# Optimization experiments

Measured on AMD Instinct MI355X. Metric: run time of the kernel, lower is better.

The kernel has to match this reference:

```python
import jax, jax.numpy as jnp
import numpy as np

D = 1024
E = 8
K = 2
NUM_ITER = 2
DT = 0.1
H = 64           # controller_hidden
CTX = 2 * D


def _gelu(t):
    return jax.nn.gelu(t, approximate=False)


def _inl(ctrl, x, v, mu):
    # ctrl: [T, 3D] -> alpha, beta, gate chunks of size D
    alpha_raw, beta_raw, gate_raw = jnp.split(ctrl, 3, axis=-1)
    alpha = jax.nn.sigmoid(alpha_raw)
    beta = jax.nn.softplus(beta_raw)
    gate = jax.nn.sigmoid(gate_raw)
    error = x - mu
    v_next = alpha * v - beta * error
    x_next = x + DT * gate * v_next
    return x_next, v_next


def setup_inputs() -> dict:
    key = jax.random.key(0)
    ks = jax.random.split(key, 20)
    s = 0.02
    inp = {
        'x': jax.random.normal(ks[0], (4, 4096, D), jnp.float32),
        # router MLP
        'w_r1': jax.random.normal(ks[1], (D, D // 4), jnp.float32) * s,
        'b_r1': jnp.zeros((D // 4,), jnp.float32),
        'w_r2': jax.random.normal(ks[2], (D // 4, E), jnp.float32) * s,
        'b_r2': jnp.zeros((E,), jnp.float32),
        # halt gate MLP
        'w_h1': jax.random.normal(ks[3], (D, D // 4), jnp.float32) * s,
        'b_h1': jnp.zeros((D // 4,), jnp.float32),
        'w_h2': jax.random.normal(ks[4], (D // 4, 1), jnp.float32) * s,
        'b_h2': jnp.zeros((1,), jnp.float32),
        # expert tables
        'expert_w1': jax.random.normal(ks[5], (E, CTX, H), jnp.float32) * s,
        'expert_b1': jnp.zeros((E, H), jnp.float32),
        'expert_w2': jax.random.normal(ks[6], (E, H, 3 * D), jnp.float32) * s,
        'expert_b2': jnp.zeros((E, 3 * D), jnp.float32),
        # shared expert
        'w_s1': jax.random.normal(ks[7], (CTX, H), jnp.float32) * s,
        'b_s1': jnp.zeros((H,), jnp.float32),
        'w_s2': jax.random.normal(ks[8], (H, 3 * D), jnp.float32) * s,
        'b_s2': jnp.zeros((3 * D,), jnp.float32),
        'shared_weight': jnp.asarray(0.5, jnp.float32),
        # refine MLP
        'w_f1': jax.random.normal(ks[9], (D, 2 * D), jnp.float32) * s,
        'b_f1': jnp.zeros((2 * D,), jnp.float32),
        'w_f2': jax.random.normal(ks[10], (2 * D, D), jnp.float32) * s,
        'b_f2': jnp.zeros((D,), jnp.float32),
        'integration_weight': jnp.full((D,), 0.5, jnp.float32),
        'mu': jnp.zeros((D,), jnp.float32),
    }
    return inp


def reference(x, w_r1, b_r1, w_r2, b_r2, w_h1, b_h1, w_h2, b_h2,
              expert_w1, expert_b1, expert_w2, expert_b2,
              w_s1, b_s1, w_s2, b_s2, shared_weight,
              w_f1, b_f1, w_f2, b_f2, integration_weight, mu):
    B, N, Dm = x.shape
    xf = x.reshape(B * N, Dm)                       # [T, D]

    # router: top-k over softmax probs, renormalized
    logits = _gelu(xf @ w_r1 + b_r1) @ w_r2 + b_r2  # [T, E]
    probs = jax.nn.softmax(logits, axis=-1)
    top_p, top_i = jax.lax.top_k(probs, K)          # [T, K]
    top_p = top_p / jnp.sum(top_p, axis=-1, keepdims=True)

    flat_idx = top_i.reshape(-1)                    # [T*K]
    flat_w = top_p.reshape(-1, 1)                   # [T*K, 1]

    v = jnp.zeros_like(xf)
    integrated = xf
    for _ in range(NUM_ITER):
        ctx = jnp.concatenate([integrated, v], axis=-1)     # [T, 2D]

        # shared expert path
        shared_ctrl = _gelu(ctx @ w_s1 + b_s1) @ w_s2 + b_s2
        x_shared, v_shared = _inl(shared_ctrl, integrated, v, mu)
        sw = jax.nn.sigmoid(shared_weight)

        # routed experts: gather per-token weights, per-token matvec
        ctx_e = jnp.repeat(ctx, K, axis=0)                  # [T*K, 2D]
        x_e = jnp.repeat(integrated, K, axis=0)
        v_e = jnp.repeat(v, K, axis=0)
        w1 = expert_w1[flat_idx]                            # [T*K, 2D, H]
        b1 = expert_b1[flat_idx]
        w2 = expert_w2[flat_idx]                            # [T*K, H, 3D]
        b2 = expert_b2[flat_idx]
        hidden = _gelu(jnp.einsum('tc,tch->th', ctx_e, w1) + b1)
        ctrl = jnp.einsum('th,tho->to', hidden, w2) + b2    # [T*K, 3D]
        x_r, v_r = _inl(ctrl, x_e, v_e, mu)
        x_r = (x_r * flat_w).reshape(B * N, K, Dm).sum(axis=1)
        v_r = (v_r * flat_w).reshape(B * N, K, Dm).sum(axis=1)

        x_next = sw * x_shared + (1.0 - sw) * x_r
        v_next = sw * v_shared + (1.0 - sw) * v_r

        halt = jax.nn.sigmoid(_gelu(x_next @ w_h1 + b_h1) @ w_h2 + b_h2)  # [T,1]
        refined = _gelu(x_next @ w_f1 + b_f1) @ w_f2 + b_f2               # [T,D]
        integrated = integrated + halt * refined * integration_weight
        v = v_next

    return integrated.reshape(B, N, Dm)
```

## Files before the change

kernel.cpp:

```cpp
#include <hip/hip_runtime.h>


#define TOK   16384
#define DDIM  1024
#define NEXP  8
#define DTC   0.1f
#define MAXDESC 512
#define NDBLK 392

using f32x4 = __attribute__((ext_vector_type(4))) float;
using bfv8  = __attribute__((ext_vector_type(8))) short;

__device__ __forceinline__ unsigned short f2bf(float x){
  unsigned u = __builtin_bit_cast(unsigned, x);
  u += 0x7fffu + ((u >> 16) & 1u);
  return (unsigned short)(u >> 16);
}
__device__ __forceinline__ float bf2f(unsigned short h){
  return __builtin_bit_cast(float, ((unsigned)h) << 16);
}
__device__ __forceinline__ float geluf(float x){
  return 0.5f * x * (1.0f + erff(x * 0.7071067811865476f));
}
__device__ __forceinline__ float sigmf(float x){ return 1.0f/(1.0f+__expf(-x)); }
__device__ __forceinline__ float softpf(float x){
  return fmaxf(x, 0.0f) + __logf(1.0f + __expf(-fabsf(x)));
}
__device__ __forceinline__ f32x4 mfma16(bfv8 a, bfv8 b, f32x4 c){
  return __builtin_amdgcn_mfma_f32_16x16x32_bf16(a, b, c, 0, 0, 0);
}
typedef __attribute__((address_space(1))) const void gvoid_t;
typedef __attribute__((address_space(3))) void svoid_t;
__device__ __forceinline__ void gload16(const void* g, void* l){
  __builtin_amdgcn_global_load_lds((gvoid_t*)g, (svoid_t*)l, 16, 0, 0);
}

__global__ __launch_bounds__(256) void transpose_cast(
    const float* __restrict__ src, unsigned short* __restrict__ dst, int R, int C)
{
  __shared__ float tile[32][33];
  size_t bo = (size_t)blockIdx.z * R * C;
  const float* s = src + bo;
  unsigned short* d = dst + bo;
  int c0 = blockIdx.x * 32, r0 = blockIdx.y * 32;
  int tx = threadIdx.x, ty = threadIdx.y;
  #pragma unroll
  for (int j = 0; j < 4; j++)
    tile[ty + 8*j][tx] = s[(size_t)(r0 + ty + 8*j) * C + c0 + tx];
  __syncthreads();
  #pragma unroll
  for (int j = 0; j < 4; j++)
    d[(size_t)(c0 + ty + 8*j) * R + r0 + tx] = f2bf(tile[tx][ty + 8*j]);
}

template<bool INIT>
__global__ __launch_bounds__(256) void ctx_k(
    const float* __restrict__ outf, unsigned short* __restrict__ ctx)
{
  const int n = TOK * 256;
  for (int i = blockIdx.x * 256 + threadIdx.x; i < n; i += gridDim.x * 256) {
    int t = i >> 8, c4 = (i & 255) * 4;
    float4 xi = ((const float4*)outf)[i];
    ushort4 xb = {f2bf(xi.x), f2bf(xi.y), f2bf(xi.z), f2bf(xi.w)};
    *(ushort4*)&ctx[(size_t)t*2048 + c4] = xb;
    if (INIT)
      *(ushort4*)&ctx[(size_t)t*2048 + 1024 + c4] = ushort4{0,0,0,0};
  }
}

template<int EPI>
__global__ __launch_bounds__(256) void gemm_k(
    const unsigned short* __restrict__ A, int lda,
    const unsigned short* __restrict__ BT,
    const float* __restrict__ bias, int Kd, int N,
    unsigned short* __restrict__ obf,
    const float* __restrict__ halt, const float* __restrict__ iw,
    float* __restrict__ integ)
{
  __shared__ unsigned short As[128][64];
  __shared__ unsigned short Bs[128][64];
  const int tid  = threadIdx.x, lane = tid & 63, w = tid >> 6;
  const int wm   = w >> 1, wn = w & 1;
  const int gm0  = blockIdx.y * 128, gn0 = blockIdx.x * 128;
  const int r8   = lane >> 3;
  const int sseg = (lane & 7) ^ r8;

  const unsigned short* aga[4];
  const unsigned short* bga[4];
  #pragma unroll
  for (int c = 0; c < 4; c++) {
    aga[c] = A  + (size_t)(gm0 + w*32 + c*8 + r8) * lda + sseg*8;
    bga[c] = BT + (size_t)(gn0 + w*32 + c*8 + r8) * Kd  + sseg*8;
  }

  f32x4 acc[4][4];
  #pragma unroll
  for (int i = 0; i < 4; i++)
    #pragma unroll
    for (int j = 0; j < 4; j++)
      acc[i][j] = f32x4{0.f,0.f,0.f,0.f};

  const int xr = (lane & 7) << 3;
  for (int k0 = 0; k0 < Kd; k0 += 64) {
    #pragma unroll
    for (int c = 0; c < 4; c++) gload16(aga[c] + k0, &As[w*32 + c*8][0]);
    #pragma unroll
    for (int c = 0; c < 4; c++) gload16(bga[c] + k0, &Bs[w*32 + c*8][0]);
    __syncthreads();
    #pragma unroll
    for (int kk = 0; kk < 64; kk += 32) {
      const int kof = kk + ((lane >> 4) << 3);
      bfv8 a[4], b[4];
      #pragma unroll
      for (int mf = 0; mf < 4; mf++)
        a[mf] = *(const bfv8*)&As[wm*64 + mf*16 + (lane & 15)][kof ^ xr];
      #pragma unroll
      for (int nf = 0; nf < 4; nf++)
        b[nf] = *(const bfv8*)&Bs[wn*64 + nf*16 + (lane & 15)][kof ^ xr];
      #pragma unroll
      for (int mf = 0; mf < 4; mf++)
        #pragma unroll
        for (int nf = 0; nf < 4; nf++)
          acc[mf][nf] = mfma16(a[mf], b[nf], acc[mf][nf]);
    }
    __syncthreads();
  }

  #pragma unroll
  for (int mf = 0; mf < 4; mf++) {
    #pragma unroll
    for (int nf = 0; nf < 4; nf++) {
      int col = gn0 + wn*64 + nf*16 + (lane & 15);
      float bc = bias[col];
      #pragma unroll
      for (int r = 0; r < 4; r++) {
        int row = gm0 + wm*64 + mf*16 + ((lane >> 4) << 2) + r;
        float v = acc[mf][nf][r] + bc;
        if (EPI == 0) {
          obf[(size_t)row * N + col] = f2bf(geluf(v));
        } else {
          integ[(size_t)row * DDIM + col] += halt[row] * v * iw[col];
        }
      }
    }
  }
}

__global__ __launch_bounds__(256) void router_k(
    const unsigned short* __restrict__ h1, const float* __restrict__ w_r2,
    const float* __restrict__ b_r2, int* __restrict__ topi, float* __restrict__ topw)
{
  int t = blockIdx.x * 4 + (threadIdx.x >> 6);
  int lane = threadIdx.x & 63;
  const unsigned short* hp = h1 + (size_t)t * 256 + lane * 4;
  float hv[4];
  #pragma unroll
  for (int j = 0; j < 4; j++) hv[j] = bf2f(hp[j]);
  float acc[8];
  #pragma unroll
  for (int e = 0; e < 8; e++) acc[e] = 0.f;
  #pragma unroll
  for (int j = 0; j < 4; j++) {
    const float* wr = w_r2 + (size_t)(lane*4 + j) * 8;
    #pragma unroll
    for (int e = 0; e < 8; e++) acc[e] += hv[j] * wr[e];
  }
  #pragma unroll
  for (int off = 32; off > 0; off >>= 1)
    #pragma unroll
    for (int e = 0; e < 8; e++) acc[e] += __shfl_xor(acc[e], off);
  if (lane == 0) {
    float lg[8];
    #pragma unroll
    for (int e = 0; e < 8; e++) lg[e] = acc[e] + b_r2[e];
    int i0 = 0; float m0 = lg[0];
    #pragma unroll
    for (int e = 1; e < 8; e++) if (lg[e] > m0) { m0 = lg[e]; i0 = e; }
    int i1 = -1; float m1 = -3.4e38f;
    #pragma unroll
    for (int e = 0; e < 8; e++) if (e != i0 && lg[e] > m1) { m1 = lg[e]; i1 = e; }
    float w0 = 1.0f / (1.0f + expf(m1 - m0));
    topi[t*2] = i0; topi[t*2+1] = i1;
    topw[t*2] = w0; topw[t*2+1] = 1.0f - w0;
  }
}

__global__ __launch_bounds__(256) void haltgate_k(
    const unsigned short* __restrict__ h1, const float* __restrict__ w_h2,
    const float* __restrict__ b_h2, float* __restrict__ halt)
{
  int t = blockIdx.x * 4 + (threadIdx.x >> 6);
  int lane = threadIdx.x & 63;
  const unsigned short* hp = h1 + (size_t)t * 256 + lane * 4;
  float s = 0.f;
  #pragma unroll
  for (int j = 0; j < 4; j++) s += bf2f(hp[j]) * w_h2[lane*4 + j];
  #pragma unroll
  for (int off = 32; off > 0; off >>= 1) s += __shfl_xor(s, off);
  if (lane == 0) halt[t] = sigmf(s + b_h2[0]);
}

__global__ __launch_bounds__(256) void bucket_k(
    const int* __restrict__ topi, int* __restrict__ cnt, int* __restrict__ slots)
{
  int g = blockIdx.x * 256 + threadIdx.x;
  int e = topi[g];
  int p = atomicAdd(&cnt[e], 1);
  slots[e * 32768 + p] = g;
}

__global__ void desc_k(const int* __restrict__ cnt, int4* __restrict__ desc,
                       int* __restrict__ ndesc)
{
  if (threadIdx.x == 0 && blockIdx.x == 0) {
    int nt = 0, hb = 0;
    for (int e = 0; e <= 8; e++) {
      int c = (e < 8) ? cnt[e] : TOK;
      for (int o = 0; o < c; o += 128) {
        int rem = c - o; if (rem > 128) rem = 128;
        desc[nt] = make_int4(e, o, rem, hb);
        nt++; hb += 128;
      }
    }
    ndesc[0] = nt;
  }
}

__global__ __launch_bounds__(256) void exp1_k(
    const unsigned short* __restrict__ ctx,
    const int4* __restrict__ desc, const int* __restrict__ ndesc,
    const int* __restrict__ slots,
    const unsigned short* __restrict__ ew1T, const float* __restrict__ eb1,
    const unsigned short* __restrict__ ws1T, const float* __restrict__ bs1,
    unsigned short* __restrict__ hiddenG)
{
  __shared__ unsigned short As[128][64];
  __shared__ unsigned short Bs[64][64];
  __shared__ int s_tok[128];
  if (blockIdx.x >= ndesc[0]) return;
  int4 dd = desc[blockIdx.x];
  const int e = dd.x, goff = dd.y, cnt = dd.z, hbase = dd.w;
  const unsigned short* w1 = (e < 8) ? ew1T + (size_t)e * 64 * 2048 : ws1T;
  const float* b1 = (e < 8) ? eb1 + e * 64 : bs1;
  const int tid = threadIdx.x, lane = tid & 63, w = tid >> 6;

  if (tid < 128) {
    int tok;
    if (e < 8) tok = (tid < cnt) ? (slots[e * 32768 + goff + tid] >> 1) : 0;
    else       tok = goff + tid;
    s_tok[tid] = tok;
  }
  __syncthreads();

  const int arow = w*8 + (lane >> 3);
  const int sseg = (lane & 7) ^ (lane >> 3);
  const unsigned short* asrc[4];
  #pragma unroll
  for (int q = 0; q < 4; q++)
    asrc[q] = ctx + (size_t)s_tok[q*32 + arow] * 2048 + sseg * 8;
  const unsigned short* bsrc[2];
  #pragma unroll
  for (int q = 0; q < 2; q++)
    bsrc[q] = w1 + (size_t)(q*32 + arow) * 2048 + sseg * 8;

  f32x4 acc[2][4];
  #pragma unroll
  for (int i = 0; i < 2; i++)
    #pragma unroll
    for (int j = 0; j < 4; j++)
      acc[i][j] = f32x4{0.f,0.f,0.f,0.f};

  const int xr = (lane & 7) << 3;
  for (int k0 = 0; k0 < 2048; k0 += 64) {
    #pragma unroll
    for (int q = 0; q < 4; q++) gload16(asrc[q] + k0, &As[q*32 + w*8][0]);
    #pragma unroll
    for (int q = 0; q < 2; q++) gload16(bsrc[q] + k0, &Bs[q*32 + w*8][0]);
    __syncthreads();
    #pragma unroll
    for (int kk = 0; kk < 64; kk += 32) {
      const int kof = kk + ((lane >> 4) << 3);
      bfv8 a[2], b[4];
      #pragma unroll
      for (int mf = 0; mf < 2; mf++)
        a[mf] = *(const bfv8*)&As[w*32 + mf*16 + (lane & 15)][kof ^ xr];
      #pragma unroll
      for (int nf = 0; nf < 4; nf++)
        b[nf] = *(const bfv8*)&Bs[nf*16 + (lane & 15)][kof ^ xr];
      #pragma unroll
      for (int mf = 0; mf < 2; mf++)
        #pragma unroll
        for (int nf = 0; nf < 4; nf++)
          acc[mf][nf] = mfma16(a[mf], b[nf], acc[mf][nf]);
    }
    __syncthreads();
  }

  #pragma unroll
  for (int mf = 0; mf < 2; mf++) {
    #pragma unroll
    for (int nf = 0; nf < 4; nf++) {
      int col = nf*16 + (lane & 15);
      float bb = b1[col];
      #pragma unroll
      for (int r = 0; r < 4; r++) {
        int row = w*32 + mf*16 + ((lane >> 4) << 2) + r;
        hiddenG[(size_t)(hbase + row) * 64 + col] = f2bf(geluf(acc[mf][nf][r] + bb));
      }
    }
  }
}

__global__ __launch_bounds__(256) void exp2_k(
    const unsigned short* __restrict__ hiddenG,
    const int4* __restrict__ desc, const int* __restrict__ ndesc,
    const int* __restrict__ slots, const float* __restrict__ topw,
    const unsigned short* __restrict__ ew2T, const float* __restrict__ eb2,
    const unsigned short* __restrict__ ws2T, const float* __restrict__ bs2,
    const float* __restrict__ swp, const float* __restrict__ mu,
    const unsigned short* __restrict__ ctx,
    unsigned* __restrict__ padPK, int dhalf)
{
  __shared__ unsigned short Hs[128][64];
  __shared__ unsigned short W2s[192][64];
  __shared__ int   s_tok[128];
  __shared__ int   s_sid[128];
  __shared__ float s_cw[128];
  if (blockIdx.x >= ndesc[0]) return;
  int4 dd = desc[blockIdx.x];
  const int e = dd.x, goff = dd.y, cnt = dd.z, hbase = dd.w;
  const unsigned short* w2 = (e < 8) ? ew2T + (size_t)e * 3072 * 64 : ws2T;
  const float* b2 = (e < 8) ? eb2 + e * 3072 : bs2;
  const int tid = threadIdx.x, lane = tid & 63, w = tid >> 6;
  const float sw = sigmf(swp[0]);

  if (tid < 128) {
    int tok = 0, sid = -1; float cw = 0.f;
    if (e < 8) {
      if (tid < cnt) { int s = slots[e*32768 + goff + tid]; tok = s >> 1; sid = s; cw = (1.f - sw) * topw[s]; }
    } else { tok = goff + tid; sid = 32768 + tok; cw = sw; }
    s_tok[tid] = tok; s_sid[tid] = sid; s_cw[tid] = cw;
  }
  const int arow = w*8 + (lane >> 3);
  const int sseg = (lane & 7) ^ (lane >> 3);
  #pragma unroll
  for (int q = 0; q < 4; q++)
    gload16(hiddenG + (size_t)(hbase + q*32 + arow) * 64 + sseg*8, &Hs[q*32 + w*8][0]);
  __syncthreads();

  const int xr = (lane & 7) << 3;
  bfv8 afr[2][2];
  #pragma unroll
  for (int mf = 0; mf < 2; mf++)
    #pragma unroll
    for (int kk = 0; kk < 2; kk++) {
      int r = w*32 + mf*16 + (lane & 15);
      int kof = kk*32 + ((lane >> 4) << 3);
      afr[mf][kk] = *(const bfv8*)&Hs[r][kof ^ xr];
    }

  for (int dc = 0; dc < 8; dc++) {
    const int d00 = dhalf * 512 + dc * 64;
    #pragma unroll
    for (int q = 0; q < 6; q++) {
      int row  = q*32 + arow;
      int grow = (row >> 6) * 1024 + d00 + (row & 63);
      gload16(w2 + (size_t)grow * 64 + sseg*8, &W2s[q*32 + w*8][0]);
    }
    __syncthreads();

    f32x4 acc[2][12];
    #pragma unroll
    for (int i = 0; i < 2; i++)
      #pragma unroll
      for (int j = 0; j < 12; j++)
        acc[i][j] = f32x4{0.f,0.f,0.f,0.f};
    #pragma unroll
    for (int kk = 0; kk < 2; kk++) {
      const int kof = kk*32 + ((lane >> 4) << 3);
      #pragma unroll
      for (int nf = 0; nf < 12; nf++) {
        bfv8 b = *(const bfv8*)&W2s[nf*16 + (lane & 15)][kof ^ xr];
        acc[0][nf] = mfma16(afr[0][kk], b, acc[0][nf]);
        acc[1][nf] = mfma16(afr[1][kk], b, acc[1][nf]);
      }
    }

    #pragma unroll
    for (int mf = 0; mf < 2; mf++) {
      #pragma unroll
      for (int cf = 0; cf < 4; cf++) {
        int d = d00 + cf*16 + (lane & 15);
        float ba = b2[d], bb = b2[1024 + d], bg = b2[2048 + d];
        float muv = mu[d];
        #pragma unroll
        for (int r = 0; r < 4; r++) {
          int row = w*32 + mf*16 + ((lane >> 4) << 2) + r;
          if (row >= cnt) continue;
          float cw = s_cw[row]; int tok = s_tok[row];
          float al = sigmf(acc[mf][cf][r] + ba);
          float be = softpf(acc[mf][4 + cf][r] + bb);
          float ga = sigmf(acc[mf][8 + cf][r] + bg);
          float xx = bf2f(ctx[(size_t)tok*2048 + d]);
          float vv = bf2f(ctx[(size_t)tok*2048 + 1024 + d]);
          float vn = al * vv - be * (xx - muv);
          unsigned pk = (unsigned)f2bf(cw * vn) | ((unsigned)f2bf(cw * ga * vn) << 16);
          padPK[(size_t)s_sid[row] * 512 + (d - dhalf*512)] = pk;
        }
      }
    }
    __syncthreads();
  }
}

__global__ __launch_bounds__(256) void combine_k(
    const unsigned* __restrict__ padPK, unsigned short* __restrict__ ctx,
    unsigned short* __restrict__ xaccB, int dhalf)
{
  const int n = TOK * 128;
  const uint4* p4 = (const uint4*)padPK;
  for (int i = blockIdx.x * 256 + threadIdx.x; i < n; i += gridDim.x * 256) {
    int t = i >> 7, j = i & 127;
    int gd = dhalf*512 + j*4;
    uint4 p0 = p4[(size_t)(2*t)       * 128 + j];
    uint4 p1 = p4[(size_t)(2*t + 1)   * 128 + j];
    uint4 ps = p4[(size_t)(32768 + t) * 128 + j];
    ushort4 xs = *(const ushort4*)&ctx[(size_t)t*2048 + gd];
    unsigned pc[4][3] = {{p0.x,p1.x,ps.x},{p0.y,p1.y,ps.y},{p0.z,p1.z,ps.z},{p0.w,p1.w,ps.w}};
    unsigned short xi[4] = {xs.x, xs.y, xs.z, xs.w};
    ushort4 xo, vo;
    unsigned short* xop = (unsigned short*)&xo;
    unsigned short* vop = (unsigned short*)&vo;
    #pragma unroll
    for (int k = 0; k < 4; k++) {
      float v  = bf2f((unsigned short)(pc[k][0] & 0xffff))
               + bf2f((unsigned short)(pc[k][1] & 0xffff))
               + bf2f((unsigned short)(pc[k][2] & 0xffff));
      float gv = bf2f((unsigned short)(pc[k][0] >> 16))
               + bf2f((unsigned short)(pc[k][1] >> 16))
               + bf2f((unsigned short)(pc[k][2] >> 16));
      float x = bf2f(xi[k]);
      xop[k] = f2bf(x + DTC * gv);
      vop[k] = f2bf(v);
    }
    *(ushort4*)&xaccB[(size_t)t*1024 + gd]      = xo;
    *(ushort4*)&ctx[(size_t)t*2048 + 1024 + gd] = vo;
  }
}

extern "C" void kernel_launch(void* const* d_in, const int* in_sizes, int n_in,
                              void* d_out, int out_size, void* d_ws, size_t ws_size,
                              hipStream_t stream)
{
  const float* x    = (const float*)d_in[0];
  const float* w_r1 = (const float*)d_in[1];
  const float* b_r1 = (const float*)d_in[2];
  const float* w_r2 = (const float*)d_in[3];
  const float* b_r2 = (const float*)d_in[4];
  const float* w_h1 = (const float*)d_in[5];
  const float* b_h1 = (const float*)d_in[6];
  const float* w_h2 = (const float*)d_in[7];
  const float* b_h2 = (const float*)d_in[8];
  const float* ew1  = (const float*)d_in[9];
  const float* eb1  = (const float*)d_in[10];
  const float* ew2  = (const float*)d_in[11];
  const float* eb2  = (const float*)d_in[12];
  const float* w_s1 = (const float*)d_in[13];
  const float* b_s1 = (const float*)d_in[14];
  const float* w_s2 = (const float*)d_in[15];
  const float* b_s2 = (const float*)d_in[16];
  const float* swt  = (const float*)d_in[17];
  const float* w_f1 = (const float*)d_in[18];
  const float* b_f1 = (const float*)d_in[19];
  const float* w_f2 = (const float*)d_in[20];
  const float* b_f2 = (const float*)d_in[21];
  const float* iw   = (const float*)d_in[22];
  const float* mu   = (const float*)d_in[23];
  float* out = (float*)d_out;

  char* ws = (char*)d_ws;
  size_t off = 0;
  auto take = [&](size_t bytes) -> char* {
    char* p = ws + off;
    off = (off + bytes + 255) & ~(size_t)255;
    return p;
  };
  const size_t TD4 = (size_t)TOK * DDIM * 4;
  unsigned short* xaccB = (unsigned short*)take((size_t)TOK * 1024 * 2);
  unsigned short* ctx   = (unsigned short*)take((size_t)TOK * 2048 * 2);
  unsigned* padPK = (unsigned*)take((size_t)49152 * 512 * 4);
  unsigned short* rh = (unsigned short*)padPK;
  unsigned short* hiddenG = (unsigned short*)take((size_t)NDBLK * 128 * 64 * 2);
  unsigned short* h1 = (unsigned short*)take((size_t)TOK * 256 * 2);
  float* halt = (float*)take((size_t)TOK * 4);
  int*   topi = (int*)take((size_t)TOK * 2 * 4);
  float* topw = (float*)take((size_t)TOK * 2 * 4);
  int*   cnt  = (int*)take(64);
  int*   ndsc = (int*)take(64);
  int4*  desc = (int4*)take((size_t)MAXDESC * 16);
  int*   slots= (int*)take((size_t)NEXP * 32768 * 4);
  unsigned short* w_r1T = (unsigned short*)take((size_t)256 * 1024 * 2);
  unsigned short* w_h1T = (unsigned short*)take((size_t)256 * 1024 * 2);
  unsigned short* w_f1T = (unsigned short*)take((size_t)2048 * 1024 * 2);
  unsigned short* w_f2T = (unsigned short*)take((size_t)1024 * 2048 * 2);
  unsigned short* w_s1T = (unsigned short*)take((size_t)64 * 2048 * 2);
  unsigned short* w_s2T = (unsigned short*)take((size_t)3072 * 64 * 2);
  unsigned short* ew1T  = (unsigned short*)take((size_t)NEXP * 64 * 2048 * 2);
  unsigned short* ew2T  = (unsigned short*)take((size_t)NEXP * 3072 * 64 * 2);
  if (off > ws_size) return;

  hipMemcpyAsync(out, x, TD4, hipMemcpyDeviceToDevice, stream);
  hipMemsetAsync(cnt, 0, 64, stream);

  dim3 tb(32, 8);
  transpose_cast<<<dim3(  8, 32, 1), tb, 0, stream>>>(w_r1, w_r1T, 1024,  256);
  transpose_cast<<<dim3(  8, 32, 1), tb, 0, stream>>>(w_h1, w_h1T, 1024,  256);
  transpose_cast<<<dim3( 64, 32, 1), tb, 0, stream>>>(w_f1, w_f1T, 1024, 2048);
  transpose_cast<<<dim3( 32, 64, 1), tb, 0, stream>>>(w_f2, w_f2T, 2048, 1024);
  transpose_cast<<<dim3(  2, 64, 1), tb, 0, stream>>>(w_s1, w_s1T, 2048,   64);
  transpose_cast<<<dim3( 96,  2, 1), tb, 0, stream>>>(w_s2, w_s2T,   64, 3072);
  transpose_cast<<<dim3(  2, 64, 8), tb, 0, stream>>>(ew1,  ew1T,  2048,   64);
  transpose_cast<<<dim3( 96,  2, 8), tb, 0, stream>>>(ew2,  ew2T,    64, 3072);

  ctx_k<true><<<2048, 256, 0, stream>>>(out, ctx);
  gemm_k<0><<<dim3(2, 128), 256, 0, stream>>>(
      ctx, 2048, w_r1T, b_r1, 1024, 256, h1, nullptr, nullptr, nullptr);
  router_k<<<TOK / 4, 256, 0, stream>>>(h1, w_r2, b_r2, topi, topw);
  bucket_k<<<TOK * 2 / 256, 256, 0, stream>>>(topi, cnt, slots);
  desc_k<<<1, 64, 0, stream>>>(cnt, desc, ndsc);

  for (int it = 0; it < 2; it++) {
    if (it > 0)
      ctx_k<false><<<2048, 256, 0, stream>>>(out, ctx);
    exp1_k<<<NDBLK, 256, 0, stream>>>(ctx, desc, ndsc, slots,
                                      ew1T, eb1, w_s1T, b_s1, hiddenG);
    for (int h = 0; h < 2; h++) {
      exp2_k<<<NDBLK, 256, 0, stream>>>(hiddenG, desc, ndsc, slots, topw,
                                        ew2T, eb2, w_s2T, b_s2, swt, mu,
                                        ctx, padPK, h);
      combine_k<<<2048, 256, 0, stream>>>(padPK, ctx, xaccB, h);
    }
    gemm_k<0><<<dim3(2, 128), 256, 0, stream>>>(
        xaccB, 1024, w_h1T, b_h1, 1024, 256, h1, nullptr, nullptr, nullptr);
    haltgate_k<<<TOK / 4, 256, 0, stream>>>(h1, w_h2, b_h2, halt);
    gemm_k<0><<<dim3(16, 128), 256, 0, stream>>>(
        xaccB, 1024, w_f1T, b_f1, 1024, 2048, rh, nullptr, nullptr, nullptr);
    gemm_k<1><<<dim3(8, 128), 256, 0, stream>>>(
        rh, 2048, w_f2T, b_f2, 2048, 1024, nullptr, halt, iw, out);
  }
}
```

Measured before the change: 1.389 ms.

## Fuse shared expert with combine, merge halt/refine GEMMs, emit ctx from epilogue

The shared-expert second layer moves into its own kernel that also does the combine step: it reads the routed padPK partials and writes xaccB and v directly, so the separate combine pass and the shared-expert padPK rows are dropped. The halt and refine first-layer weights are concatenated so one GEMM (EPI 2) writes both outputs. The refine-output GEMM epilogue now writes the bf16 copy of the updated state into ctx, which removes the per-iteration ctx_k pass. A block-index swizzle is also added to gemm_k to improve L2 locality. The cost is more scattered epilogue loads in the fused shared kernel.

After: 1.557 ms. +12.1%, slower.

```diff
diff --git a/kernel.cpp b/kernel.cpp
--- a/kernel.cpp
+++ b/kernel.cpp
@@ -7,6 +7,7 @@
 #define DTC   0.1f
 #define MAXDESC 512
 #define NDBLK 392
+#define SHBASE 33664
 
 using f32x4 = __attribute__((ext_vector_type(4))) float;
 using bfv8  = __attribute__((ext_vector_type(8))) short;
@@ -53,7 +54,6 @@
     d[(size_t)(c0 + ty + 8*j) * R + r0 + tx] = f2bf(tile[tx][ty + 8*j]);
 }
 
-template<bool INIT>
 __global__ __launch_bounds__(256) void ctx_k(
     const float* __restrict__ outf, unsigned short* __restrict__ ctx)
 {
@@ -63,8 +63,7 @@
     float4 xi = ((const float4*)outf)[i];
     ushort4 xb = {f2bf(xi.x), f2bf(xi.y), f2bf(xi.z), f2bf(xi.w)};
     *(ushort4*)&ctx[(size_t)t*2048 + c4] = xb;
-    if (INIT)
-      *(ushort4*)&ctx[(size_t)t*2048 + 1024 + c4] = ushort4{0,0,0,0};
+    *(ushort4*)&ctx[(size_t)t*2048 + 1024 + c4] = ushort4{0,0,0,0};
   }
 }
 
@@ -72,16 +71,22 @@
 __global__ __launch_bounds__(256) void gemm_k(
     const unsigned short* __restrict__ A, int lda,
     const unsigned short* __restrict__ BT,
-    const float* __restrict__ bias, int Kd, int N,
-    unsigned short* __restrict__ obf,
+    const float* __restrict__ bias, const float* __restrict__ bias2,
+    int Kd, int N,
+    unsigned short* __restrict__ obf, unsigned short* __restrict__ obf2,
     const float* __restrict__ halt, const float* __restrict__ iw,
-    float* __restrict__ integ)
+    float* __restrict__ integ, unsigned short* __restrict__ ctxX)
 {
   __shared__ unsigned short As[128][64];
   __shared__ unsigned short Bs[128][64];
+  const int total = gridDim.x * gridDim.y;
+  const int bid = blockIdx.y * gridDim.x + blockIdx.x;
+  const int swz = (bid & 7) * (total >> 3) + (bid >> 3);
+  const int bx = swz % gridDim.x, by = swz / gridDim.x;
+
   const int tid  = threadIdx.x, lane = tid & 63, w = tid >> 6;
   const int wm   = w >> 1, wn = w & 1;
-  const int gm0  = blockIdx.y * 128, gn0 = blockIdx.x * 128;
+  const int gm0  = by * 128, gn0 = bx * 128;
   const int r8   = lane >> 3;
   const int sseg = (lane & 7) ^ r8;
 
@@ -131,15 +136,23 @@
     #pragma unroll
     for (int nf = 0; nf < 4; nf++) {
       int col = gn0 + wn*64 + nf*16 + (lane & 15);
-      float bc = bias[col];
+      float bc;
+      if (EPI == 2) bc = (col < 2048) ? bias[col] : bias2[col - 2048];
+      else          bc = bias[col];
       #pragma unroll
       for (int r = 0; r < 4; r++) {
         int row = gm0 + wm*64 + mf*16 + ((lane >> 4) << 2) + r;
         float v = acc[mf][nf][r] + bc;
         if (EPI == 0) {
           obf[(size_t)row * N + col] = f2bf(geluf(v));
+        } else if (EPI == 2) {
+          if (col < 2048) obf [(size_t)row * 2048 + col]        = f2bf(geluf(v));
+          else            obf2[(size_t)row * 256 + (col - 2048)] = f2bf(geluf(v));
         } else {
-          integ[(size_t)row * DDIM + col] += halt[row] * v * iw[col];
+          size_t ix = (size_t)row * DDIM + col;
+          float nv = integ[ix] + halt[row] * v * iw[col];
+          integ[ix] = nv;
+          ctxX[(size_t)row * 2048 + col] = f2bf(nv);
         }
       }
     }
@@ -214,13 +227,17 @@
 {
   if (threadIdx.x == 0 && blockIdx.x == 0) {
     int nt = 0, hb = 0;
-    for (int e = 0; e <= 8; e++) {
-      int c = (e < 8) ? cnt[e] : TOK;
+    for (int e = 0; e < NEXP; e++) {
+      int c = cnt[e];
       for (int o = 0; o < c; o += 128) {
         int rem = c - o; if (rem > 128) rem = 128;
         desc[nt] = make_int4(e, o, rem, hb);
         nt++; hb += 128;
       }
+    }
+    for (int o = 0; o < TOK; o += 128) {
+      desc[nt] = make_int4(8, o, 128, SHBASE + o);
+      nt++;
     }
     ndesc[0] = nt;
   }
@@ -311,12 +328,11 @@
   }
 }
 
-__global__ __launch_bounds__(256) void exp2_k(
+__global__ __launch_bounds__(256) void exp2r_k(
     const unsigned short* __restrict__ hiddenG,
     const int4* __restrict__ desc, const int* __restrict__ ndesc,
     const int* __restrict__ slots, const float* __restrict__ topw,
     const unsigned short* __restrict__ ew2T, const float* __restrict__ eb2,
-    const unsigned short* __restrict__ ws2T, const float* __restrict__ bs2,
     const float* __restrict__ swp, const float* __restrict__ mu,
     const unsigned short* __restrict__ ctx,
     unsigned* __restrict__ padPK, int dhalf)
@@ -329,16 +345,15 @@
   if (blockIdx.x >= ndesc[0]) return;
   int4 dd = desc[blockIdx.x];
   const int e = dd.x, goff = dd.y, cnt = dd.z, hbase = dd.w;
-  const unsigned short* w2 = (e < 8) ? ew2T + (size_t)e * 3072 * 64 : ws2T;
-  const float* b2 = (e < 8) ? eb2 + e * 3072 : bs2;
+  if (e >= 8) return;
+  const unsigned short* w2 = ew2T + (size_t)e * 3072 * 64;
+  const float* b2 = eb2 + e * 3072;
   const int tid = threadIdx.x, lane = tid & 63, w = tid >> 6;
   const float sw = sigmf(swp[0]);
 
   if (tid < 128) {
-    int tok = 0, sid = -1; float cw = 0.f;
-    if (e < 8) {
-      if (tid < cnt) { int s = slots[e*32768 + goff + tid]; tok = s >> 1; sid = s; cw = (1.f - sw) * topw[s]; }
-    } else { tok = goff + tid; sid = 32768 + tok; cw = sw; }
+    int tok = 0, sid = 0; float cw = 0.f;
+    if (tid < cnt) { int s = slots[e*32768 + goff + tid]; tok = s >> 1; sid = s; cw = (1.f - sw) * topw[s]; }
     s_tok[tid] = tok; s_sid[tid] = sid; s_cw[tid] = cw;
   }
   const int arow = w*8 + (lane >> 3);
@@ -413,38 +428,96 @@
   }
 }
 
-__global__ __launch_bounds__(256) void combine_k(
-    const unsigned* __restrict__ padPK, unsigned short* __restrict__ ctx,
+__global__ __launch_bounds__(256) void exp2sc_k(
+    const unsigned short* __restrict__ hiddenG,
+    const unsigned short* __restrict__ ws2T, const float* __restrict__ bs2,
+    const float* __restrict__ swp, const float* __restrict__ mu,
+    unsigned short* __restrict__ ctx,
+    const unsigned* __restrict__ padPK,
     unsigned short* __restrict__ xaccB, int dhalf)
 {
-  const int n = TOK * 128;
-  const uint4* p4 = (const uint4*)padPK;
-  for (int i = blockIdx.x * 256 + threadIdx.x; i < n; i += gridDim.x * 256) {
-    int t = i >> 7, j = i & 127;
-    int gd = dhalf*512 + j*4;
-    uint4 p0 = p4[(size_t)(2*t)       * 128 + j];
-    uint4 p1 = p4[(size_t)(2*t + 1)   * 128 + j];
-    uint4 ps = p4[(size_t)(32768 + t) * 128 + j];
-    ushort4 xs = *(const ushort4*)&ctx[(size_t)t*2048 + gd];
-    unsigned pc[4][3] = {{p0.x,p1.x,ps.x},{p0.y,p1.y,ps.y},{p0.z,p1.z,ps.z},{p0.w,p1.w,ps.w}};
-    unsigned short xi[4] = {xs.x, xs.y, xs.z, xs.w};
-    ushort4 xo, vo;
-    unsigned short* xop = (unsigned short*)&xo;
-    unsigned short* vop = (unsigned short*)&vo;
-    #pragma unroll
-    for (int k = 0; k < 4; k++) {
-      float v  = bf2f((unsigned short)(pc[k][0] & 0xffff))
-               + bf2f((unsigned short)(pc[k][1] & 0xffff))
-               + bf2f((unsigned short)(pc[k][2] & 0xffff));
-      float gv = bf2f((unsigned short)(pc[k][0] >> 16))
-               + bf2f((unsigned short)(pc[k][1] >> 16))
-               + bf2f((unsigned short)(pc[k][2] >> 16));
-      float x = bf2f(xi[k]);
-      xop[k] = f2bf(x + DTC * gv);
-      vop[k] = f2bf(v);
-    }
-    *(ushort4*)&xaccB[(size_t)t*1024 + gd]      = xo;
-    *(ushort4*)&ctx[(size_t)t*2048 + 1024 + gd] = vo;
+  __shared__ unsigned short Hs[128][64];
+  __shared__ unsigned short W2s[192][64];
+  const int tid = threadIdx.x, lane = tid & 63, w = tid >> 6;
+  const int tbase = blockIdx.x * 128;
+  const float sw = sigmf(swp[0]);
+
+  const int arow = w*8 + (lane >> 3);
+  const int sseg = (lane & 7) ^ (lane >> 3);
+  #pragma unroll
+  for (int q = 0; q < 4; q++)
+    gload16(hiddenG + (size_t)(SHBASE + tbase + q*32 + arow) * 64 + sseg*8,
+            &Hs[q*32 + w*8][0]);
+  __syncthreads();
+
+  const int xr = (lane & 7) << 3;
+  bfv8 afr[2][2];
+  #pragma unroll
+  for (int mf = 0; mf < 2; mf++)
+    #pragma unroll
+    for (int kk = 0; kk < 2; kk++) {
+      int r = w*32 + mf*16 + (lane & 15);
+      int kof = kk*32 + ((lane >> 4) << 3);
+      afr[mf][kk] = *(const bfv8*)&Hs[r][kof ^ xr];
+    }
+
+  for (int dc = 0; dc < 8; dc++) {
+    const int d00 = dhalf * 512 + dc * 64;
+    #pragma unroll
+    for (int q = 0; q < 6; q++) {
+      int row  = q*32 + arow;
+      int grow = (row >> 6) * 1024 + d00 + (row & 63);
+      gload16(ws2T + (size_t)grow * 64 + sseg*8, &W2s[q*32 + w*8][0]);
+    }
+    __syncthreads();
+
+    f32x4 acc[2][12];
+    #pragma unroll
+    for (int i = 0; i < 2; i++)
+      #pragma unroll
+      for (int j = 0; j < 12; j++)
+        acc[i][j] = f32x4{0.f,0.f,0.f,0.f};
+    #pragma unroll
+    for (int kk = 0; kk < 2; kk++) {
+      const int kof = kk*32 + ((lane >> 4) << 3);
+      #pragma unroll
+      for (int nf = 0; nf < 12; nf++) {
+        bfv8 b = *(const bfv8*)&W2s[nf*16 + (lane & 15)][kof ^ xr];
+        acc[0][nf] = mfma16(afr[0][kk], b, acc[0][nf]);
+        acc[1][nf] = mfma16(afr[1][kk], b, acc[1][nf]);
+      }
+    }
+
+    #pragma unroll
+    for (int mf = 0; mf < 2; mf++) {
+      #pragma unroll
+      for (int cf = 0; cf < 4; cf++) {
+        int d = d00 + cf*16 + (lane & 15);
+        int dl = d - dhalf*512;
+        float ba = bs2[d], bb = bs2[1024 + d], bg = bs2[2048 + d];
+        float muv = mu[d];
+        #pragma unroll
+        for (int r = 0; r < 4; r++) {
+          int row = w*32 + mf*16 + ((lane >> 4) << 2) + r;
+          int tok = tbase + row;
+          float al = sigmf(acc[mf][cf][r] + ba);
+          float be = softpf(acc[mf][4 + cf][r] + bb);
+          float ga = sigmf(acc[mf][8 + cf][r] + bg);
+          float xx = bf2f(ctx[(size_t)tok*2048 + d]);
+          float vv = bf2f(ctx[(size_t)tok*2048 + 1024 + d]);
+          float vn = al * vv - be * (xx - muv);
+          unsigned pk0 = padPK[(size_t)(2*tok)     * 512 + dl];
+          unsigned pk1 = padPK[(size_t)(2*tok + 1) * 512 + dl];
+          float vtot  = sw * vn      + bf2f((unsigned short)(pk0 & 0xffff))
+                                     + bf2f((unsigned short)(pk1 & 0xffff));
+          float gvtot = sw * ga * vn + bf2f((unsigned short)(pk0 >> 16))
+                                     + bf2f((unsigned short)(pk1 >> 16));
+          xaccB[(size_t)tok*1024 + d]        = f2bf(xx + DTC * gvtot);
+          ctx[(size_t)tok*2048 + 1024 + d]   = f2bf(vtot);
+        }
+      }
+    }
+    __syncthreads();
   }
 }
 
@@ -488,9 +561,9 @@
   const size_t TD4 = (size_t)TOK * DDIM * 4;
   unsigned short* xaccB = (unsigned short*)take((size_t)TOK * 1024 * 2);
   unsigned short* ctx   = (unsigned short*)take((size_t)TOK * 2048 * 2);
-  unsigned* padPK = (unsigned*)take((size_t)49152 * 512 * 4);
+  unsigned* padPK = (unsigned*)take((size_t)32768 * 512 * 4);
   unsigned short* rh = (unsigned short*)padPK;
-  unsigned short* hiddenG = (unsigned short*)take((size_t)NDBLK * 128 * 64 * 2);
+  unsigned short* hiddenG = (unsigned short*)take((size_t)(SHBASE + TOK) * 64 * 2);
   unsigned short* h1 = (unsigned short*)take((size_t)TOK * 256 * 2);
   float* halt = (float*)take((size_t)TOK * 4);
   int*   topi = (int*)take((size_t)TOK * 2 * 4);
@@ -500,8 +573,7 @@
   int4*  desc = (int4*)take((size_t)MAXDESC * 16);
   int*   slots= (int*)take((size_t)NEXP * 32768 * 4);
   unsigned short* w_r1T = (unsigned short*)take((size_t)256 * 1024 * 2);
-  unsigned short* w_h1T = (unsigned short*)take((size_t)256 * 1024 * 2);
-  unsigned short* w_f1T = (unsigned short*)take((size_t)2048 * 1024 * 2);
+  unsigned short* wFH   = (unsigned short*)take((size_t)2304 * 1024 * 2);
   unsigned short* w_f2T = (unsigned short*)take((size_t)1024 * 2048 * 2);
   unsigned short* w_s1T = (unsigned short*)take((size_t)64 * 2048 * 2);
   unsigned short* w_s2T = (unsigned short*)take((size_t)3072 * 64 * 2);
@@ -514,38 +586,37 @@
 
   dim3 tb(32, 8);
   transpose_cast<<<dim3(  8, 32, 1), tb, 0, stream>>>(w_r1, w_r1T, 1024,  256);
-  transpose_cast<<<dim3(  8, 32, 1), tb, 0, stream>>>(w_h1, w_h1T, 1024,  256);
-  transpose_cast<<<dim3( 64, 32, 1), tb, 0, stream>>>(w_f1, w_f1T, 1024, 2048);
+  transpose_cast<<<dim3( 64, 32, 1), tb, 0, stream>>>(w_f1, wFH, 1024, 2048);
+  transpose_cast<<<dim3(  8, 32, 1), tb, 0, stream>>>(w_h1, wFH + (size_t)2048*1024, 1024, 256);
   transpose_cast<<<dim3( 32, 64, 1), tb, 0, stream>>>(w_f2, w_f2T, 2048, 1024);
   transpose_cast<<<dim3(  2, 64, 1), tb, 0, stream>>>(w_s1, w_s1T, 2048,   64);
   transpose_cast<<<dim3( 96,  2, 1), tb, 0, stream>>>(w_s2, w_s2T,   64, 3072);
   transpose_cast<<<dim3(  2, 64, 8), tb, 0, stream>>>(ew1,  ew1T,  2048,   64);
   transpose_cast<<<dim3( 96,  2, 8), tb, 0, stream>>>(ew2,  ew2T,    64, 3072);
 
-  ctx_k<true><<<2048, 256, 0, stream>>>(out, ctx);
+  ctx_k<<<2048, 256, 0, stream>>>(out, ctx);
   gemm_k<0><<<dim3(2, 128), 256, 0, stream>>>(
-      ctx, 2048, w_r1T, b_r1, 1024, 256, h1, nullptr, nullptr, nullptr);
+      ctx, 2048, w_r1T, b_r1, nullptr, 1024, 256, h1, nullptr,
+      nullptr, nullptr, nullptr, nullptr);
   router_k<<<TOK / 4, 256, 0, stream>>>(h1, w_r2, b_r2, topi, topw);
   bucket_k<<<TOK * 2 / 256, 256, 0, stream>>>(topi, cnt, slots);
   desc_k<<<1, 64, 0, stream>>>(cnt, desc, ndsc);
 
   for (int it = 0; it < 2; it++) {
-    if (it > 0)
-      ctx_k<false><<<2048, 256, 0, stream>>>(out, ctx);
     exp1_k<<<NDBLK, 256, 0, stream>>>(ctx, desc, ndsc, slots,
                                       ew1T, eb1, w_s1T, b_s1, hiddenG);
     for (int h = 0; h < 2; h++) {
-      exp2_k<<<NDBLK, 256, 0, stream>>>(hiddenG, desc, ndsc, slots, topw,
-                                        ew2T, eb2, w_s2T, b_s2, swt, mu,
-                                        ctx, padPK, h);
-      combine_k<<<2048, 256, 0, stream>>>(padPK, ctx, xaccB, h);
-    }
-    gemm_k<0><<<dim3(2, 128), 256, 0, stream>>>(
-        xaccB, 1024, w_h1T, b_h1, 1024, 256, h1, nullptr, nullptr, nullptr);
+      exp2r_k<<<NDBLK, 256, 0, stream>>>(hiddenG, desc, ndsc, slots, topw,
+                                         ew2T, eb2, swt, mu, ctx, padPK, h);
+      exp2sc_k<<<TOK / 128, 256, 0, stream>>>(hiddenG, w_s2T, b_s2, swt, mu,
+                                              ctx, padPK, xaccB, h);
+    }
+    gemm_k<2><<<dim3(18, 128), 256, 0, stream>>>(
+        xaccB, 1024, wFH, b_f1, b_h1, 1024, 2304, rh, h1,
+        nullptr, nullptr, nullptr, nullptr);
     haltgate_k<<<TOK / 4, 256, 0, stream>>>(h1, w_h2, b_h2, halt);
-    gemm_k<0><<<dim3(16, 128), 256, 0, stream>>>(
-        xaccB, 1024, w_f1T, b_f1, 1024, 2048, rh, nullptr, nullptr, nullptr);
     gemm_k<1><<<dim3(8, 128), 256, 0, stream>>>(
-        rh, 2048, w_f2T, b_f2, 2048, 1024, nullptr, halt, iw, out);
-  }
-}
+        rh, 2048, w_f2T, b_f2, nullptr, 2048, 1024, nullptr, nullptr,
+        halt, iw, out, ctx);
+  }
+}
```
